# Performance work log

Hardware: AMD Instinct MI355X
Metric: run time of the kernel (lower is better)

The kernel has to match this reference:

```python
import jax, jax.numpy as jnp
import numpy as np

N_AGENTS = 16
OBS_DIM = 256
ACT_DIM = 32
B, T = 16, 64
ADAPTIVE = max(10, N_AGENTS)  # 16 Monte-Carlo counterfactual samples
H1, H2 = 128, 64


def setup_inputs() -> dict:
    key = jax.random.key(0)
    ks = jax.random.split(key, 10)
    in_dim = OBS_DIM + ACT_DIM
    inp = {
        "obs": jax.random.normal(ks[0], (B, T, N_AGENTS, OBS_DIM), dtype=jnp.float32),
        "actions": jax.random.uniform(ks[1], (B, T, N_AGENTS, ACT_DIM), dtype=jnp.float32),
        "cf_actions": jax.random.uniform(ks[2], (N_AGENTS, ADAPTIVE, B, T, ACT_DIM), dtype=jnp.float32),
        "W1": jax.random.normal(ks[3], (in_dim, H1), dtype=jnp.float32) / np.sqrt(in_dim),
        "b1": jnp.zeros((H1,), dtype=jnp.float32),
        "W2": jax.random.normal(ks[4], (H1, H2), dtype=jnp.float32) / np.sqrt(H1),
        "b2": jnp.zeros((H2,), dtype=jnp.float32),
        "W3": jax.random.normal(ks[5], (H2, ACT_DIM), dtype=jnp.float32) / np.sqrt(H2),
        "b3": jnp.zeros((ACT_DIM,), dtype=jnp.float32),
    }
    return inp


def _mlp(x, W1, b1, W2, b2, W3, b3):
    h = jax.nn.relu(x @ W1 + b1)
    h = jax.nn.relu(h @ W2 + b2)
    return h @ W3 + b3


def reference(obs, actions, cf_actions, W1, b1, W2, b2, W3, b3):
    # obs: [B,T,N,D], actions: [B,T,N,A], cf_actions: [N,S,B,T,A]
    obs_n = jnp.moveaxis(obs, 2, 0)      # [N,B,T,D]
    act_n = jnp.moveaxis(actions, 2, 0)  # [N,B,T,A]

    # p(with k): MLP([obs_k, action_k]) for all agents at once  -> [N,B,T,A]
    p_with = _mlp(jnp.concatenate([obs_n, act_n], axis=-1), W1, b1, W2, b2, W3, b3)
    # p(zero action)
    p_zero = _mlp(jnp.concatenate([obs_n, jnp.zeros_like(act_n)], axis=-1),
                  W1, b1, W2, b2, W3, b3)
    # Monte-Carlo counterfactuals: [N,S,B,T,A]
    S = cf_actions.shape[1]
    obs_rep = jnp.broadcast_to(obs_n[:, None], (obs_n.shape[0], S) + obs_n.shape[1:])
    p_cf = _mlp(jnp.concatenate([obs_rep, cf_actions], axis=-1), W1, b1, W2, b2, W3, b3)

    p_without = (p_zero + p_cf.sum(axis=1)) / (S + 1)  # [N,B,T,A]

    # F.kl_div(log_softmax(p_with), softmax(p_without), reduction='none')
    log_p = jax.nn.log_softmax(p_with, axis=-1)
    q = jax.nn.softmax(p_without, axis=-1)
    log_q = jax.nn.log_softmax(p_without, axis=-1)
    kl = q * (log_q - log_p)  # [N,B,T,A]

    # stack over agents on last dim then mean over action dim -> [B,T,N]
    influences = jnp.moveaxis(kl.mean(axis=-1), 0, -1)
    return influences
```

## Files before the change

### kernel.cpp

```cpp
#include <hip/hip_runtime.h>

#define NAG   16
#define OBSD  256
#define ACTD  32
#define BB    16
#define TT    64
#define SCF   16
#define H1D   128
#define H2D   64
#define BT    (BB*TT)
#define NTOK  (BT*NAG)
#define NEVAL 18

typedef float f4 __attribute__((ext_vector_type(4)));

__global__ __launch_bounds__(256) void k_h1obs(
    const float* __restrict__ obs, const float* __restrict__ W1,
    const float* __restrict__ b1, float* __restrict__ h1obs)
{
    __shared__ float As[32][36];
    __shared__ float Bs[32 * 128];

    const int tid = threadIdx.x;
    const int g0  = blockIdx.x * 32;
    const int rb  = tid >> 5;
    const int cb  = tid & 31;
    const int r0  = rb * 4;
    const int c0  = cb * 4;
    const int arow = tid >> 3;
    const int akk  = (tid & 7) * 4;

    float acc[4][4] = {};

    for (int kt = 0; kt < OBSD; kt += 32) {
        f4 av = *(const f4*)(obs + (g0 + arow) * OBSD + kt + akk);
        *(f4*)(&As[arow][akk]) = av;
        const float* wsrc = W1 + kt * H1D;
        #pragma unroll
        for (int u = 0; u < 4; ++u) {
            f4 bv = *(const f4*)(wsrc + u * 1024 + tid * 4);
            *(f4*)(Bs + u * 1024 + tid * 4) = bv;
        }
        __syncthreads();
        #pragma unroll
        for (int k0 = 0; k0 < 32; k0 += 4) {
            f4 a[4], b[4];
            #pragma unroll
            for (int i = 0; i < 4; ++i) a[i] = *(const f4*)(&As[r0 + i][k0]);
            #pragma unroll
            for (int kk = 0; kk < 4; ++kk) b[kk] = *(const f4*)(Bs + (k0 + kk) * H1D + c0);
            #pragma unroll
            for (int i = 0; i < 4; ++i)
                #pragma unroll
                for (int kk = 0; kk < 4; ++kk)
                    #pragma unroll
                    for (int j = 0; j < 4; ++j)
                        acc[i][j] = fmaf(a[i][kk], b[kk][j], acc[i][j]);
        }
        __syncthreads();
    }

    f4 bias = *(const f4*)(b1 + c0);
    #pragma unroll
    for (int i = 0; i < 4; ++i) {
        f4 v;
        #pragma unroll
        for (int j = 0; j < 4; ++j) v[j] = acc[i][j] + bias[j];
        *(f4*)(h1obs + (g0 + r0 + i) * H1D + c0) = v;
    }
}

__global__ __launch_bounds__(256) void k_main(
    const float* __restrict__ actions, const float* __restrict__ cf,
    const float* __restrict__ W1, const float* __restrict__ W2,
    const float* __restrict__ b2v, const float* __restrict__ W3,
    const float* __restrict__ b3v, const float* __restrict__ h1obs,
    float* __restrict__ out)
{
    __shared__ float Acts[32][36];
    __shared__ float W1s[32 * 128];
    __shared__ float W2s[128 * 64];
    __shared__ float Hs[32][132];
    __shared__ float H2s[32][68];

    const int tid = threadIdx.x;
    const int g0  = blockIdx.x * 32;

    const int rb1 = tid >> 5, cb1 = tid & 31;
    const int rb2 = tid >> 4, cb2 = tid & 15;
    const int r3 = tid >> 3, cb3 = tid & 7;

    #pragma unroll
    for (int u = 0; u < 4; ++u)
        *(f4*)(W1s + u * 1024 + tid * 4) =
            *(const f4*)(W1 + OBSD * H1D + u * 1024 + tid * 4);
    #pragma unroll
    for (int u = 0; u < 8; ++u)
        *(f4*)(W2s + u * 1024 + tid * 4) =
            *(const f4*)(W2 + u * 1024 + tid * 4);

    f4 hobs[4];
    #pragma unroll
    for (int i = 0; i < 4; ++i)
        hobs[i] = *(const f4*)(h1obs + (g0 + rb1 * 4 + i) * H1D + cb1 * 4);

    f4 bias2 = *(const f4*)(b2v + cb2 * 4);
    f4 bias3 = *(const f4*)(b3v + cb3 * 4);

    const int atok = tid >> 3;
    const int aa   = (tid & 7) * 4;
    const int g_at = g0 + atok;
    const int n_at = g_at & (NAG - 1);
    const int bt_at = g_at >> 4;

    f4 pw = {0.f, 0.f, 0.f, 0.f};
    f4 pq = {0.f, 0.f, 0.f, 0.f};

    __syncthreads();

    for (int e = 0; e < NEVAL; ++e) {
        if (e != 1) {
            const float* src;
            if (e == 0) src = actions + g_at * ACTD + aa;
            else        src = cf + ((n_at * SCF + (e - 2)) * BT + bt_at) * ACTD + aa;
            f4 v = *(const f4*)src;
            *(f4*)(&Acts[atok][aa]) = v;
        }
        __syncthreads();

        f4 hval[4];
        if (e != 1) {
            float acc[4][4] = {};
            #pragma unroll
            for (int k0 = 0; k0 < ACTD; k0 += 4) {
                f4 a[4], b[4];
                #pragma unroll
                for (int i = 0; i < 4; ++i) a[i] = *(const f4*)(&Acts[rb1 * 4 + i][k0]);
                #pragma unroll
                for (int kk = 0; kk < 4; ++kk) b[kk] = *(const f4*)(W1s + (k0 + kk) * H1D + cb1 * 4);
                #pragma unroll
                for (int i = 0; i < 4; ++i)
                    #pragma unroll
                    for (int kk = 0; kk < 4; ++kk)
                        #pragma unroll
                        for (int j = 0; j < 4; ++j)
                            acc[i][j] = fmaf(a[i][kk], b[kk][j], acc[i][j]);
            }
            #pragma unroll
            for (int i = 0; i < 4; ++i)
                #pragma unroll
                for (int j = 0; j < 4; ++j)
                    hval[i][j] = fmaxf(hobs[i][j] + acc[i][j], 0.f);
        } else {
            #pragma unroll
            for (int i = 0; i < 4; ++i)
                #pragma unroll
                for (int j = 0; j < 4; ++j)
                    hval[i][j] = fmaxf(hobs[i][j], 0.f);
        }
        #pragma unroll
        for (int i = 0; i < 4; ++i)
            *(f4*)(&Hs[rb1 * 4 + i][cb1 * 4]) = hval[i];
        __syncthreads();

        {
            float acc[2][4] = {};
            #pragma unroll 8
            for (int k0 = 0; k0 < H1D; k0 += 4) {
                f4 a0 = *(const f4*)(&Hs[rb2 * 2][k0]);
                f4 a1 = *(const f4*)(&Hs[rb2 * 2 + 1][k0]);
                f4 b[4];
                #pragma unroll
                for (int kk = 0; kk < 4; ++kk) b[kk] = *(const f4*)(W2s + (k0 + kk) * H2D + cb2 * 4);
                #pragma unroll
                for (int kk = 0; kk < 4; ++kk)
                    #pragma unroll
                    for (int j = 0; j < 4; ++j) {
                        acc[0][j] = fmaf(a0[kk], b[kk][j], acc[0][j]);
                        acc[1][j] = fmaf(a1[kk], b[kk][j], acc[1][j]);
                    }
            }
            #pragma unroll
            for (int i = 0; i < 2; ++i) {
                f4 v;
                #pragma unroll
                for (int j = 0; j < 4; ++j) v[j] = fmaxf(acc[i][j] + bias2[j], 0.f);
                *(f4*)(&H2s[rb2 * 2 + i][cb2 * 4]) = v;
            }
        }
        __syncthreads();

        {
            f4 acc = {0.f, 0.f, 0.f, 0.f};
            #pragma unroll 8
            for (int k0 = 0; k0 < H2D; k0 += 4) {
                f4 a = *(const f4*)(&H2s[r3][k0]);
                #pragma unroll
                for (int kk = 0; kk < 4; ++kk) {
                    f4 b = *(const f4*)(W3 + (k0 + kk) * ACTD + cb3 * 4);
                    #pragma unroll
                    for (int j = 0; j < 4; ++j)
                        acc[j] = fmaf(a[kk], b[j], acc[j]);
                }
            }
            #pragma unroll
            for (int j = 0; j < 4; ++j) acc[j] += bias3[j];
            if (e == 0) pw = acc;
            else {
                #pragma unroll
                for (int j = 0; j < 4; ++j) pq[j] += acc[j];
            }
        }
    }

    const float inv17 = 1.0f / 17.0f;
    f4 qv;
    #pragma unroll
    for (int j = 0; j < 4; ++j) qv[j] = pq[j] * inv17;

    float mw = fmaxf(fmaxf(pw[0], pw[1]), fmaxf(pw[2], pw[3]));
    float mq = fmaxf(fmaxf(qv[0], qv[1]), fmaxf(qv[2], qv[3]));
    #pragma unroll
    for (int m = 1; m < 8; m <<= 1) {
        mw = fmaxf(mw, __shfl_xor(mw, m));
        mq = fmaxf(mq, __shfl_xor(mq, m));
    }
    float sw = 0.f, sq = 0.f;
    #pragma unroll
    for (int j = 0; j < 4; ++j) {
        sw += expf(pw[j] - mw);
        sq += expf(qv[j] - mq);
    }
    #pragma unroll
    for (int m = 1; m < 8; m <<= 1) {
        sw += __shfl_xor(sw, m);
        sq += __shfl_xor(sq, m);
    }
    const float lsw = logf(sw), lsq = logf(sq);
    float kl = 0.f;
    #pragma unroll
    for (int j = 0; j < 4; ++j) {
        float lq = qv[j] - mq - lsq;
        float lp = pw[j] - mw - lsw;
        float q  = expf(lq);
        kl += q * (lq - lp);
    }
    #pragma unroll
    for (int m = 1; m < 8; m <<= 1) kl += __shfl_xor(kl, m);

    if (cb3 == 0) out[g0 + r3] = kl * (1.0f / 32.0f);
}

extern "C" void kernel_launch(void* const* d_in, const int* in_sizes, int n_in,
                              void* d_out, int out_size, void* d_ws, size_t ws_size,
                              hipStream_t stream)
{
    const float* obs     = (const float*)d_in[0];
    const float* actions = (const float*)d_in[1];
    const float* cf      = (const float*)d_in[2];
    const float* W1      = (const float*)d_in[3];
    const float* b1      = (const float*)d_in[4];
    const float* W2      = (const float*)d_in[5];
    const float* b2      = (const float*)d_in[6];
    const float* W3      = (const float*)d_in[7];
    const float* b3      = (const float*)d_in[8];
    float* outp  = (float*)d_out;
    float* h1obs = (float*)d_ws;

    k_h1obs<<<NTOK / 32, 256, 0, stream>>>(obs, W1, b1, h1obs);
    k_main <<<NTOK / 32, 256, 0, stream>>>(actions, cf, W1, W2, b2, W3, b3,
                                           h1obs, outp);
}
```

Measured before the change: 259.4 us.

## Fuse obs layer into main MLP kernel and split evaluations across two blocks

Folds the obs-projection GEMM into the main kernel, dropping the h1obs workspace round trip, and splits the 18 MLP evaluations across two blocks per token tile. Partial sums go to workspace and a small new kernel finishes the KL. LDS shrinks to 40KB by streaming W2 in halves and using XOR-swizzled H tiles, so launch_bounds asks for 4 blocks per CU. In exchange the obs GEMM runs twice per tile, W1 and W3 are read from global memory, and each evaluation gains extra W2 reloads and barriers.

```diff
diff --git a/kernel.cpp b/kernel.cpp
--- a/kernel.cpp
+++ b/kernel.cpp
@@ -3,52 +3,62 @@
 #define NAG   16
 #define OBSD  256
 #define ACTD  32
-#define BB    16
-#define TT    64
 #define SCF   16
 #define H1D   128
 #define H2D   64
-#define BT    (BB*TT)
-#define NTOK  (BT*NAG)
-#define NEVAL 18
+#define BT    1024
+#define NTOK  16384
+#define CFS   32768
 
 typedef float f4 __attribute__((ext_vector_type(4)));
 
-__global__ __launch_bounds__(256) void k_h1obs(
-    const float* __restrict__ obs, const float* __restrict__ W1,
-    const float* __restrict__ b1, float* __restrict__ h1obs)
+#define HS_OFF   0
+#define H2S_OFF  4096
+#define W2S_OFF  6144
+
+#define WS_PW   0
+#define WS_PQ0  524288
+#define WS_PQ1  1048576
+
+__global__ __launch_bounds__(256, 4) void k_fused(
+    const float* __restrict__ obs, const float* __restrict__ actions,
+    const float* __restrict__ cf, const float* __restrict__ W1,
+    const float* __restrict__ b1, const float* __restrict__ W2,
+    const float* __restrict__ b2v, const float* __restrict__ W3,
+    const float* __restrict__ b3v, float* __restrict__ ws)
 {
-    __shared__ float As[32][36];
-    __shared__ float Bs[32 * 128];
-
-    const int tid = threadIdx.x;
-    const int g0  = blockIdx.x * 32;
-    const int rb  = tid >> 5;
-    const int cb  = tid & 31;
-    const int r0  = rb * 4;
-    const int c0  = cb * 4;
-    const int arow = tid >> 3;
-    const int akk  = (tid & 7) * 4;
-
-    float acc[4][4] = {};
-
-    for (int kt = 0; kt < OBSD; kt += 32) {
-        f4 av = *(const f4*)(obs + (g0 + arow) * OBSD + kt + akk);
-        *(f4*)(&As[arow][akk]) = av;
-        const float* wsrc = W1 + kt * H1D;
-        #pragma unroll
-        for (int u = 0; u < 4; ++u) {
-            f4 bv = *(const f4*)(wsrc + u * 1024 + tid * 4);
-            *(f4*)(Bs + u * 1024 + tid * 4) = bv;
-        }
-        __syncthreads();
-        #pragma unroll
-        for (int k0 = 0; k0 < 32; k0 += 4) {
+    __shared__ float lds[10240];
+
+    const int tid   = threadIdx.x;
+    const int chunk = blockIdx.x & 1;
+    const int g0    = (blockIdx.x >> 1) * 32;
+
+    const int rb1 = tid >> 5, cb1 = tid & 31;
+    const int rb2 = tid >> 4, cb2 = tid & 15;
+    const int r3  = tid >> 3, cb3 = tid & 7;
+
+    {
+        const float* src = obs + g0 * OBSD;
+        #pragma unroll
+        for (int j = 0; j < 8; ++j) {
+            int idx = tid + j * 256;
+            *(f4*)(lds + idx * 4) = *(const f4*)(src + idx * 4);
+        }
+    }
+    __syncthreads();
+
+    f4 hobs[4];
+    {
+        float acc[4][4] = {};
+        #pragma unroll 8
+        for (int k = 0; k < OBSD; k += 4) {
             f4 a[4], b[4];
             #pragma unroll
-            for (int i = 0; i < 4; ++i) a[i] = *(const f4*)(&As[r0 + i][k0]);
-            #pragma unroll
-            for (int kk = 0; kk < 4; ++kk) b[kk] = *(const f4*)(Bs + (k0 + kk) * H1D + c0);
+            for (int i = 0; i < 4; ++i)
+                a[i] = *(const f4*)(lds + (rb1 * 4 + i) * OBSD + k);
+            #pragma unroll
+            for (int kk = 0; kk < 4; ++kk)
+                b[kk] = *(const f4*)(W1 + (k + kk) * H1D + cb1 * 4);
             #pragma unroll
             for (int i = 0; i < 4; ++i)
                 #pragma unroll
@@ -57,87 +67,55 @@
                     for (int j = 0; j < 4; ++j)
                         acc[i][j] = fmaf(a[i][kk], b[kk][j], acc[i][j]);
         }
-        __syncthreads();
-    }
-
-    f4 bias = *(const f4*)(b1 + c0);
+        f4 bias = *(const f4*)(b1 + cb1 * 4);
+        #pragma unroll
+        for (int i = 0; i < 4; ++i)
+            #pragma unroll
+            for (int j = 0; j < 4; ++j)
+                hobs[i][j] = acc[i][j] + bias[j];
+    }
+    __syncthreads();
+
+    int aoff[4], cfoff[4];
     #pragma unroll
     for (int i = 0; i < 4; ++i) {
-        f4 v;
-        #pragma unroll
-        for (int j = 0; j < 4; ++j) v[j] = acc[i][j] + bias[j];
-        *(f4*)(h1obs + (g0 + r0 + i) * H1D + c0) = v;
-    }
-}
-
-__global__ __launch_bounds__(256) void k_main(
-    const float* __restrict__ actions, const float* __restrict__ cf,
-    const float* __restrict__ W1, const float* __restrict__ W2,
-    const float* __restrict__ b2v, const float* __restrict__ W3,
-    const float* __restrict__ b3v, const float* __restrict__ h1obs,
-    float* __restrict__ out)
-{
-    __shared__ float Acts[32][36];
-    __shared__ float W1s[32 * 128];
-    __shared__ float W2s[128 * 64];
-    __shared__ float Hs[32][132];
-    __shared__ float H2s[32][68];
-
-    const int tid = threadIdx.x;
-    const int g0  = blockIdx.x * 32;
-
-    const int rb1 = tid >> 5, cb1 = tid & 31;
-    const int rb2 = tid >> 4, cb2 = tid & 15;
-    const int r3 = tid >> 3, cb3 = tid & 7;
-
-    #pragma unroll
-    for (int u = 0; u < 4; ++u)
-        *(f4*)(W1s + u * 1024 + tid * 4) =
-            *(const f4*)(W1 + OBSD * H1D + u * 1024 + tid * 4);
-    #pragma unroll
-    for (int u = 0; u < 8; ++u)
-        *(f4*)(W2s + u * 1024 + tid * 4) =
-            *(const f4*)(W2 + u * 1024 + tid * 4);
-
-    f4 hobs[4];
-    #pragma unroll
-    for (int i = 0; i < 4; ++i)
-        hobs[i] = *(const f4*)(h1obs + (g0 + rb1 * 4 + i) * H1D + cb1 * 4);
-
+        int tg = g0 + rb1 * 4 + i;
+        aoff[i]  = tg * ACTD;
+        cfoff[i] = ((tg & (NAG - 1)) * SCF * BT + (tg >> 4)) * ACTD;
+    }
+    const float* W1a = W1 + OBSD * H1D;
     f4 bias2 = *(const f4*)(b2v + cb2 * 4);
     f4 bias3 = *(const f4*)(b3v + cb3 * 4);
 
-    const int atok = tid >> 3;
-    const int aa   = (tid & 7) * 4;
-    const int g_at = g0 + atok;
-    const int n_at = g_at & (NAG - 1);
-    const int bt_at = g_at >> 4;
-
     f4 pw = {0.f, 0.f, 0.f, 0.f};
     f4 pq = {0.f, 0.f, 0.f, 0.f};
 
-    __syncthreads();
-
-    for (int e = 0; e < NEVAL; ++e) {
-        if (e != 1) {
-            const float* src;
-            if (e == 0) src = actions + g_at * ACTD + aa;
-            else        src = cf + ((n_at * SCF + (e - 2)) * BT + bt_at) * ACTD + aa;
-            f4 v = *(const f4*)src;
-            *(f4*)(&Acts[atok][aa]) = v;
-        }
-        __syncthreads();
-
-        f4 hval[4];
-        if (e != 1) {
+    const int xt1[4] = { ((rb1*4+0)&7)<<2, ((rb1*4+1)&7)<<2,
+                         ((rb1*4+2)&7)<<2, ((rb1*4+3)&7)<<2 };
+    const int t20 = rb2 * 2, t21 = rb2 * 2 + 1;
+    const int x20 = (t20 & 7) << 2, x21 = (t21 & 7) << 2;
+    const int x3  = (r3 & 7) << 2;
+
+    for (int ee = 0; ee < 9; ++ee) {
+        const bool zeroEval = (chunk == 1) && (ee == 0);
+        const bool withEval = (chunk == 0) && (ee == 0);
+        const int  s        = (chunk == 0) ? (ee - 1) : (ee + 7);
+
+        f4 hv[4];
+        if (!zeroEval) {
+            const float* ap[4];
+            #pragma unroll
+            for (int i = 0; i < 4; ++i)
+                ap[i] = withEval ? (actions + aoff[i]) : (cf + cfoff[i] + s * CFS);
             float acc[4][4] = {};
             #pragma unroll
-            for (int k0 = 0; k0 < ACTD; k0 += 4) {
+            for (int k = 0; k < ACTD; k += 4) {
                 f4 a[4], b[4];
                 #pragma unroll
-                for (int i = 0; i < 4; ++i) a[i] = *(const f4*)(&Acts[rb1 * 4 + i][k0]);
-                #pragma unroll
-                for (int kk = 0; kk < 4; ++kk) b[kk] = *(const f4*)(W1s + (k0 + kk) * H1D + cb1 * 4);
+                for (int i = 0; i < 4; ++i) a[i] = *(const f4*)(ap[i] + k);
+                #pragma unroll
+                for (int kk = 0; kk < 4; ++kk)
+                    b[kk] = *(const f4*)(W1a + (k + kk) * H1D + cb1 * 4);
                 #pragma unroll
                 for (int i = 0; i < 4; ++i)
                     #pragma unroll
@@ -150,54 +128,88 @@
             for (int i = 0; i < 4; ++i)
                 #pragma unroll
                 for (int j = 0; j < 4; ++j)
-                    hval[i][j] = fmaxf(hobs[i][j] + acc[i][j], 0.f);
+                    hv[i][j] = fmaxf(hobs[i][j] + acc[i][j], 0.f);
         } else {
             #pragma unroll
             for (int i = 0; i < 4; ++i)
                 #pragma unroll
                 for (int j = 0; j < 4; ++j)
-                    hval[i][j] = fmaxf(hobs[i][j], 0.f);
-        }
-        #pragma unroll
-        for (int i = 0; i < 4; ++i)
-            *(f4*)(&Hs[rb1 * 4 + i][cb1 * 4]) = hval[i];
+                    hv[i][j] = fmaxf(hobs[i][j], 0.f);
+        }
+
+        #pragma unroll
+        for (int j = 0; j < 4; ++j)
+            *(f4*)(lds + W2S_OFF + tid * 4 + j * 1024) =
+                *(const f4*)(W2 + tid * 4 + j * 1024);
+
+        #pragma unroll
+        for (int i = 0; i < 4; ++i) {
+            int t = rb1 * 4 + i;
+            *(f4*)(lds + HS_OFF + t * H1D + ((cb1 * 4) ^ xt1[i])) = hv[i];
+        }
         __syncthreads();
 
+        float acc2[2][4] = {};
+        #pragma unroll 8
+        for (int k = 0; k < 64; k += 4) {
+            f4 a0 = *(const f4*)(lds + HS_OFF + t20 * H1D + (k ^ x20));
+            f4 a1 = *(const f4*)(lds + HS_OFF + t21 * H1D + (k ^ x21));
+            f4 b[4];
+            #pragma unroll
+            for (int kk = 0; kk < 4; ++kk)
+                b[kk] = *(const f4*)(lds + W2S_OFF + (k + kk) * H2D + cb2 * 4);
+            #pragma unroll
+            for (int kk = 0; kk < 4; ++kk)
+                #pragma unroll
+                for (int j = 0; j < 4; ++j) {
+                    acc2[0][j] = fmaf(a0[kk], b[kk][j], acc2[0][j]);
+                    acc2[1][j] = fmaf(a1[kk], b[kk][j], acc2[1][j]);
+                }
+        }
+        __syncthreads();
+
+        #pragma unroll
+        for (int j = 0; j < 4; ++j)
+            *(f4*)(lds + W2S_OFF + tid * 4 + j * 1024) =
+                *(const f4*)(W2 + 4096 + tid * 4 + j * 1024);
+        __syncthreads();
+
+        #pragma unroll 8
+        for (int k = 0; k < 64; k += 4) {
+            f4 a0 = *(const f4*)(lds + HS_OFF + t20 * H1D + ((64 + k) ^ x20));
+            f4 a1 = *(const f4*)(lds + HS_OFF + t21 * H1D + ((64 + k) ^ x21));
+            f4 b[4];
+            #pragma unroll
+            for (int kk = 0; kk < 4; ++kk)
+                b[kk] = *(const f4*)(lds + W2S_OFF + (k + kk) * H2D + cb2 * 4);
+            #pragma unroll
+            for (int kk = 0; kk < 4; ++kk)
+                #pragma unroll
+                for (int j = 0; j < 4; ++j) {
+                    acc2[0][j] = fmaf(a0[kk], b[kk][j], acc2[0][j]);
+                    acc2[1][j] = fmaf(a1[kk], b[kk][j], acc2[1][j]);
+                }
+        }
         {
-            float acc[2][4] = {};
-            #pragma unroll 8
-            for (int k0 = 0; k0 < H1D; k0 += 4) {
-                f4 a0 = *(const f4*)(&Hs[rb2 * 2][k0]);
-                f4 a1 = *(const f4*)(&Hs[rb2 * 2 + 1][k0]);
-                f4 b[4];
-                #pragma unroll
-                for (int kk = 0; kk < 4; ++kk) b[kk] = *(const f4*)(W2s + (k0 + kk) * H2D + cb2 * 4);
-                #pragma unroll
-                for (int kk = 0; kk < 4; ++kk)
-                    #pragma unroll
-                    for (int j = 0; j < 4; ++j) {
-                        acc[0][j] = fmaf(a0[kk], b[kk][j], acc[0][j]);
-                        acc[1][j] = fmaf(a1[kk], b[kk][j], acc[1][j]);
-                    }
+            f4 v0, v1;
+            #pragma unroll
+            for (int j = 0; j < 4; ++j) {
+                v0[j] = fmaxf(acc2[0][j] + bias2[j], 0.f);
+                v1[j] = fmaxf(acc2[1][j] + bias2[j], 0.f);
             }
-            #pragma unroll
-            for (int i = 0; i < 2; ++i) {
-                f4 v;
-                #pragma unroll
-                for (int j = 0; j < 4; ++j) v[j] = fmaxf(acc[i][j] + bias2[j], 0.f);
-                *(f4*)(&H2s[rb2 * 2 + i][cb2 * 4]) = v;
-            }
+            *(f4*)(lds + H2S_OFF + t20 * H2D + ((cb2 * 4) ^ x20)) = v0;
+            *(f4*)(lds + H2S_OFF + t21 * H2D + ((cb2 * 4) ^ x21)) = v1;
         }
         __syncthreads();
 
         {
             f4 acc = {0.f, 0.f, 0.f, 0.f};
             #pragma unroll 8
-            for (int k0 = 0; k0 < H2D; k0 += 4) {
-                f4 a = *(const f4*)(&H2s[r3][k0]);
+            for (int k = 0; k < H2D; k += 4) {
+                f4 a = *(const f4*)(lds + H2S_OFF + r3 * H2D + (k ^ x3));
                 #pragma unroll
                 for (int kk = 0; kk < 4; ++kk) {
-                    f4 b = *(const f4*)(W3 + (k0 + kk) * ACTD + cb3 * 4);
+                    f4 b = *(const f4*)(W3 + (k + kk) * ACTD + cb3 * 4);
                     #pragma unroll
                     for (int j = 0; j < 4; ++j)
                         acc[j] = fmaf(a[kk], b[j], acc[j]);
@@ -205,7 +217,7 @@
             }
             #pragma unroll
             for (int j = 0; j < 4; ++j) acc[j] += bias3[j];
-            if (e == 0) pw = acc;
+            if (withEval) pw = acc;
             else {
                 #pragma unroll
                 for (int j = 0; j < 4; ++j) pq[j] += acc[j];
@@ -213,10 +225,30 @@
         }
     }
 
+    const int gg = g0 + r3;
+    if (chunk == 0) {
+        *(f4*)(ws + WS_PW  + gg * ACTD + cb3 * 4) = pw;
+        *(f4*)(ws + WS_PQ0 + gg * ACTD + cb3 * 4) = pq;
+    } else {
+        *(f4*)(ws + WS_PQ1 + gg * ACTD + cb3 * 4) = pq;
+    }
+}
+
+__global__ __launch_bounds__(256) void k_kl(
+    const float* __restrict__ ws, float* __restrict__ out)
+{
+    const int tid = threadIdx.x;
+    const int gg  = blockIdx.x * 32 + (tid >> 3);
+    const int cb3 = tid & 7;
+
+    f4 pw  = *(const f4*)(ws + WS_PW  + gg * ACTD + cb3 * 4);
+    f4 pa  = *(const f4*)(ws + WS_PQ0 + gg * ACTD + cb3 * 4);
+    f4 pb  = *(const f4*)(ws + WS_PQ1 + gg * ACTD + cb3 * 4);
+
     const float inv17 = 1.0f / 17.0f;
     f4 qv;
     #pragma unroll
-    for (int j = 0; j < 4; ++j) qv[j] = pq[j] * inv17;
+    for (int j = 0; j < 4; ++j) qv[j] = (pa[j] + pb[j]) * inv17;
 
     float mw = fmaxf(fmaxf(pw[0], pw[1]), fmaxf(pw[2], pw[3]));
     float mq = fmaxf(fmaxf(qv[0], qv[1]), fmaxf(qv[2], qv[3]));
@@ -242,13 +274,12 @@
     for (int j = 0; j < 4; ++j) {
         float lq = qv[j] - mq - lsq;
         float lp = pw[j] - mw - lsw;
-        float q  = expf(lq);
-        kl += q * (lq - lp);
+        kl += expf(lq) * (lq - lp);
     }
     #pragma unroll
     for (int m = 1; m < 8; m <<= 1) kl += __shfl_xor(kl, m);
 
-    if (cb3 == 0) out[g0 + r3] = kl * (1.0f / 32.0f);
+    if (cb3 == 0) out[gg] = kl * (1.0f / 32.0f);
 }
 
 extern "C" void kernel_launch(void* const* d_in, const int* in_sizes, int n_in,
@@ -264,10 +295,10 @@
     const float* b2      = (const float*)d_in[6];
     const float* W3      = (const float*)d_in[7];
     const float* b3      = (const float*)d_in[8];
-    float* outp  = (float*)d_out;
-    float* h1obs = (float*)d_ws;
-
-    k_h1obs<<<NTOK / 32, 256, 0, stream>>>(obs, W1, b1, h1obs);
-    k_main <<<NTOK / 32, 256, 0, stream>>>(actions, cf, W1, W2, b2, W3, b3,
-                                           h1obs, outp);
+    float* outp = (float*)d_out;
+    float* ws   = (float*)d_ws;
+
+    k_fused<<<(NTOK / 32) * 2, 256, 0, stream>>>(obs, actions, cf, W1, b1, W2,
+                                                 b2, W3, b3, ws);
+    k_kl  <<<NTOK / 32, 256, 0, stream>>>(ws, outp);
 }
```

After: 434.5 us. 67.5% more time.

## Fuse obs-projection GEMM into main MLP kernel with a shared LDS union

Applied to the files above, without the earlier changes.

Merges the two kernels into one, so the first-layer obs projection stays in registers and is no longer written to and re-read from a workspace buffer. The whole 32x256 obs tile is staged in LDS up front, and the same LDS buffer is reused, in aliased regions, for the evaluation loop's activations and weights. It adds launch_bounds(256,2) and an extra barrier per iteration, which may constrain registers, and it removes one kernel launch.

```diff
diff --git a/kernel.cpp b/kernel.cpp
--- a/kernel.cpp
+++ b/kernel.cpp
@@ -3,52 +3,68 @@
 #define NAG   16
 #define OBSD  256
 #define ACTD  32
-#define BB    16
-#define TT    64
 #define SCF   16
 #define H1D   128
 #define H2D   64
-#define BT    (BB*TT)
-#define NTOK  (BT*NAG)
+#define BT    1024
+#define NTOK  16384
+#define CFS   32768
 #define NEVAL 18
 
 typedef float f4 __attribute__((ext_vector_type(4)));
 
-__global__ __launch_bounds__(256) void k_h1obs(
-    const float* __restrict__ obs, const float* __restrict__ W1,
-    const float* __restrict__ b1, float* __restrict__ h1obs)
+#define OBS_OFF  0
+#define BS_OFF   8192
+#define ACT_OFF  0
+#define W1S_OFF  1152
+#define W2S_OFF  5248
+#define HS_OFF   13440
+#define H2S_OFF  17664
+#define LDS_FLOATS 19840
+
+__global__ __launch_bounds__(256, 2) void k_fused(
+    const float* __restrict__ obs, const float* __restrict__ actions,
+    const float* __restrict__ cf, const float* __restrict__ W1,
+    const float* __restrict__ b1, const float* __restrict__ W2,
+    const float* __restrict__ b2v, const float* __restrict__ W3,
+    const float* __restrict__ b3v, float* __restrict__ out)
 {
-    __shared__ float As[32][36];
-    __shared__ float Bs[32 * 128];
+    __shared__ float lds[LDS_FLOATS];
 
     const int tid = threadIdx.x;
     const int g0  = blockIdx.x * 32;
-    const int rb  = tid >> 5;
-    const int cb  = tid & 31;
-    const int r0  = rb * 4;
-    const int c0  = cb * 4;
-    const int arow = tid >> 3;
-    const int akk  = (tid & 7) * 4;
+
+    const int rb1 = tid >> 5, cb1 = tid & 31;
+    const int rb2 = tid >> 4, cb2 = tid & 15;
+    const int r3  = tid >> 3, cb3 = tid & 7;
+
+    {
+        const float* src = obs + g0 * OBSD;
+        #pragma unroll
+        for (int j = 0; j < 8; ++j) {
+            int idx = tid + j * 256;
+            *(f4*)(lds + OBS_OFF + idx * 4) = *(const f4*)(src + idx * 4);
+        }
+    }
 
     float acc[4][4] = {};
-
     for (int kt = 0; kt < OBSD; kt += 32) {
-        f4 av = *(const f4*)(obs + (g0 + arow) * OBSD + kt + akk);
-        *(f4*)(&As[arow][akk]) = av;
+        __syncthreads();
         const float* wsrc = W1 + kt * H1D;
         #pragma unroll
-        for (int u = 0; u < 4; ++u) {
-            f4 bv = *(const f4*)(wsrc + u * 1024 + tid * 4);
-            *(f4*)(Bs + u * 1024 + tid * 4) = bv;
-        }
+        for (int u = 0; u < 4; ++u)
+            *(f4*)(lds + BS_OFF + u * 1024 + tid * 4) =
+                *(const f4*)(wsrc + u * 1024 + tid * 4);
         __syncthreads();
         #pragma unroll
         for (int k0 = 0; k0 < 32; k0 += 4) {
             f4 a[4], b[4];
             #pragma unroll
-            for (int i = 0; i < 4; ++i) a[i] = *(const f4*)(&As[r0 + i][k0]);
-            #pragma unroll
-            for (int kk = 0; kk < 4; ++kk) b[kk] = *(const f4*)(Bs + (k0 + kk) * H1D + c0);
+            for (int i = 0; i < 4; ++i)
+                a[i] = *(const f4*)(lds + OBS_OFF + (rb1 * 4 + i) * OBSD + kt + k0);
+            #pragma unroll
+            for (int kk = 0; kk < 4; ++kk)
+                b[kk] = *(const f4*)(lds + BS_OFF + (k0 + kk) * H1D + cb1 * 4);
             #pragma unroll
             for (int i = 0; i < 4; ++i)
                 #pragma unroll
@@ -57,52 +73,26 @@
                     for (int j = 0; j < 4; ++j)
                         acc[i][j] = fmaf(a[i][kk], b[kk][j], acc[i][j]);
         }
-        __syncthreads();
-    }
-
-    f4 bias = *(const f4*)(b1 + c0);
-    #pragma unroll
-    for (int i = 0; i < 4; ++i) {
-        f4 v;
-        #pragma unroll
-        for (int j = 0; j < 4; ++j) v[j] = acc[i][j] + bias[j];
-        *(f4*)(h1obs + (g0 + r0 + i) * H1D + c0) = v;
-    }
-}
-
-__global__ __launch_bounds__(256) void k_main(
-    const float* __restrict__ actions, const float* __restrict__ cf,
-    const float* __restrict__ W1, const float* __restrict__ W2,
-    const float* __restrict__ b2v, const float* __restrict__ W3,
-    const float* __restrict__ b3v, const float* __restrict__ h1obs,
-    float* __restrict__ out)
-{
-    __shared__ float Acts[32][36];
-    __shared__ float W1s[32 * 128];
-    __shared__ float W2s[128 * 64];
-    __shared__ float Hs[32][132];
-    __shared__ float H2s[32][68];
-
-    const int tid = threadIdx.x;
-    const int g0  = blockIdx.x * 32;
-
-    const int rb1 = tid >> 5, cb1 = tid & 31;
-    const int rb2 = tid >> 4, cb2 = tid & 15;
-    const int r3 = tid >> 3, cb3 = tid & 7;
+    }
+    f4 hobs[4];
+    {
+        f4 bias = *(const f4*)(b1 + cb1 * 4);
+        #pragma unroll
+        for (int i = 0; i < 4; ++i)
+            #pragma unroll
+            for (int j = 0; j < 4; ++j)
+                hobs[i][j] = acc[i][j] + bias[j];
+    }
+    __syncthreads();
 
     #pragma unroll
     for (int u = 0; u < 4; ++u)
-        *(f4*)(W1s + u * 1024 + tid * 4) =
+        *(f4*)(lds + W1S_OFF + u * 1024 + tid * 4) =
             *(const f4*)(W1 + OBSD * H1D + u * 1024 + tid * 4);
     #pragma unroll
     for (int u = 0; u < 8; ++u)
-        *(f4*)(W2s + u * 1024 + tid * 4) =
+        *(f4*)(lds + W2S_OFF + u * 1024 + tid * 4) =
             *(const f4*)(W2 + u * 1024 + tid * 4);
-
-    f4 hobs[4];
-    #pragma unroll
-    for (int i = 0; i < 4; ++i)
-        hobs[i] = *(const f4*)(h1obs + (g0 + rb1 * 4 + i) * H1D + cb1 * 4);
 
     f4 bias2 = *(const f4*)(b2v + cb2 * 4);
     f4 bias3 = *(const f4*)(b3v + cb3 * 4);
@@ -122,95 +112,100 @@
         if (e != 1) {
             const float* src;
             if (e == 0) src = actions + g_at * ACTD + aa;
-            else        src = cf + ((n_at * SCF + (e - 2)) * BT + bt_at) * ACTD + aa;
-            f4 v = *(const f4*)src;
-            *(f4*)(&Acts[atok][aa]) = v;
-        }
-        __syncthreads();
-
-        f4 hval[4];
+            else        src = cf + (n_at * SCF + (e - 2)) * CFS + bt_at * ACTD + aa;
+            *(f4*)(lds + ACT_OFF + atok * 36 + aa) = *(const f4*)src;
+        }
+        __syncthreads();
+
+        f4 hv[4];
         if (e != 1) {
-            float acc[4][4] = {};
+            float a1c[4][4] = {};
             #pragma unroll
             for (int k0 = 0; k0 < ACTD; k0 += 4) {
                 f4 a[4], b[4];
                 #pragma unroll
-                for (int i = 0; i < 4; ++i) a[i] = *(const f4*)(&Acts[rb1 * 4 + i][k0]);
-                #pragma unroll
-                for (int kk = 0; kk < 4; ++kk) b[kk] = *(const f4*)(W1s + (k0 + kk) * H1D + cb1 * 4);
+                for (int i = 0; i < 4; ++i)
+                    a[i] = *(const f4*)(lds + ACT_OFF + (rb1 * 4 + i) * 36 + k0);
+                #pragma unroll
+                for (int kk = 0; kk < 4; ++kk)
+                    b[kk] = *(const f4*)(lds + W1S_OFF + (k0 + kk) * H1D + cb1 * 4);
                 #pragma unroll
                 for (int i = 0; i < 4; ++i)
                     #pragma unroll
                     for (int kk = 0; kk < 4; ++kk)
                         #pragma unroll
                         for (int j = 0; j < 4; ++j)
-                            acc[i][j] = fmaf(a[i][kk], b[kk][j], acc[i][j]);
+                            a1c[i][j] = fmaf(a[i][kk], b[kk][j], a1c[i][j]);
             }
             #pragma unroll
             for (int i = 0; i < 4; ++i)
                 #pragma unroll
                 for (int j = 0; j < 4; ++j)
-                    hval[i][j] = fmaxf(hobs[i][j] + acc[i][j], 0.f);
+                    hv[i][j] = fmaxf(hobs[i][j] + a1c[i][j], 0.f);
         } else {
             #pragma unroll
             for (int i = 0; i < 4; ++i)
                 #pragma unroll
                 for (int j = 0; j < 4; ++j)
-                    hval[i][j] = fmaxf(hobs[i][j], 0.f);
+                    hv[i][j] = fmaxf(hobs[i][j], 0.f);
         }
         #pragma unroll
         for (int i = 0; i < 4; ++i)
-            *(f4*)(&Hs[rb1 * 4 + i][cb1 * 4]) = hval[i];
+            *(f4*)(lds + HS_OFF + (rb1 * 4 + i) * 132 + cb1 * 4) = hv[i];
         __syncthreads();
 
         {
-            float acc[2][4] = {};
+            float acc2[2][4] = {};
+            const int t0 = rb2 * 2, t1 = rb2 * 2 + 1;
             #pragma unroll 8
             for (int k0 = 0; k0 < H1D; k0 += 4) {
-                f4 a0 = *(const f4*)(&Hs[rb2 * 2][k0]);
-                f4 a1 = *(const f4*)(&Hs[rb2 * 2 + 1][k0]);
+                f4 a0 = *(const f4*)(lds + HS_OFF + t0 * 132 + k0);
+                f4 a1 = *(const f4*)(lds + HS_OFF + t1 * 132 + k0);
                 f4 b[4];
                 #pragma unroll
-                for (int kk = 0; kk < 4; ++kk) b[kk] = *(const f4*)(W2s + (k0 + kk) * H2D + cb2 * 4);
+                for (int kk = 0; kk < 4; ++kk)
+                    b[kk] = *(const f4*)(lds + W2S_OFF + (k0 + kk) * H2D + cb2 * 4);
                 #pragma unroll
                 for (int kk = 0; kk < 4; ++kk)
                     #pragma unroll
                     for (int j = 0; j < 4; ++j) {
-                        acc[0][j] = fmaf(a0[kk], b[kk][j], acc[0][j]);
-                        acc[1][j] = fmaf(a1[kk], b[kk][j], acc[1][j]);
+                        acc2[0][j] = fmaf(a0[kk], b[kk][j], acc2[0][j]);
+                        acc2[1][j] = fmaf(a1[kk], b[kk][j], acc2[1][j]);
                     }
             }
-            #pragma unroll
-            for (int i = 0; i < 2; ++i) {
-                f4 v;
-                #pragma unroll
-                for (int j = 0; j < 4; ++j) v[j] = fmaxf(acc[i][j] + bias2[j], 0.f);
-                *(f4*)(&H2s[rb2 * 2 + i][cb2 * 4]) = v;
-            }
+            f4 v0, v1;
+            #pragma unroll
+            for (int j = 0; j < 4; ++j) {
+                v0[j] = fmaxf(acc2[0][j] + bias2[j], 0.f);
+                v1[j] = fmaxf(acc2[1][j] + bias2[j], 0.f);
+            }
+            *(f4*)(lds + H2S_OFF + t0 * 68 + cb2 * 4) = v0;
+            *(f4*)(lds + H2S_OFF + t1 * 68 + cb2 * 4) = v1;
         }
         __syncthreads();
 
         {
-            f4 acc = {0.f, 0.f, 0.f, 0.f};
+            f4 a3 = {0.f, 0.f, 0.f, 0.f};
             #pragma unroll 8
             for (int k0 = 0; k0 < H2D; k0 += 4) {
-                f4 a = *(const f4*)(&H2s[r3][k0]);
+                f4 a = *(const f4*)(lds + H2S_OFF + r3 * 68 + k0);
                 #pragma unroll
                 for (int kk = 0; kk < 4; ++kk) {
                     f4 b = *(const f4*)(W3 + (k0 + kk) * ACTD + cb3 * 4);
                     #pragma unroll
                     for (int j = 0; j < 4; ++j)
-                        acc[j] = fmaf(a[kk], b[j], acc[j]);
+                        a3[j] = fmaf(a[kk], b[j], a3[j]);
                 }
             }
             #pragma unroll
-            for (int j = 0; j < 4; ++j) acc[j] += bias3[j];
-            if (e == 0) pw = acc;
+            for (int j = 0; j < 4; ++j) a3[j] += bias3[j];
+            if (e == 0) pw = a3;
             else {
                 #pragma unroll
-                for (int j = 0; j < 4; ++j) pq[j] += acc[j];
-            }
-        }
+                for (int j = 0; j < 4; ++j) pq[j] += a3[j];
+            }
+        }
+        __syncthreads();
     }
 
     const float inv17 = 1.0f / 17.0f;
@@ -242,8 +237,7 @@
     for (int j = 0; j < 4; ++j) {
         float lq = qv[j] - mq - lsq;
         float lp = pw[j] - mw - lsw;
-        float q  = expf(lq);
-        kl += q * (lq - lp);
+        kl += expf(lq) * (lq - lp);
     }
     #pragma unroll
     for (int m = 1; m < 8; m <<= 1) kl += __shfl_xor(kl, m);
@@ -264,10 +258,8 @@
     const float* b2      = (const float*)d_in[6];
     const float* W3      = (const float*)d_in[7];
     const float* b3      = (const float*)d_in[8];
-    float* outp  = (float*)d_out;
-    float* h1obs = (float*)d_ws;
-
-    k_h1obs<<<NTOK / 32, 256, 0, stream>>>(obs, W1, b1, h1obs);
-    k_main <<<NTOK / 32, 256, 0, stream>>>(actions, cf, W1, W2, b2, W3, b3,
-                                           h1obs, outp);
+    float* outp = (float*)d_out;
+
+    k_fused<<<NTOK / 32, 256, 0, stream>>>(obs, actions, cf, W1, b1, W2,
+                                           b2, W3, b3, outp);
 }
```

Result: slower. 265.1 us (+2.2%).
